# Kernel optimization log

Hardware: AMD Instinct MI355X
Metric: run time of the kernel (lower is better)

The kernel has to match this reference:

```python
import jax, jax.numpy as jnp
import numpy as np

EPS = 1e-6
ROPE_THETA = 10000.0
NH, NKV, HD = 32, 8, 128  # num_heads, num_kv_heads, head_dim


def rmsnorm(x, w):
    # normalize over last dim (head_dim), matching per-head RMSNorm
    return x * jax.lax.rsqrt(jnp.mean(x * x, axis=-1, keepdims=True) + EPS) * w


def rope(x):
    # torchtune-style interleaved RoPE. x: [b, s, h, d]
    b, s, h, d = x.shape
    half = d // 2
    freqs = 1.0 / (ROPE_THETA ** (jnp.arange(0, d, 2, dtype=jnp.float32) / d))  # [d/2]
    ang = jnp.arange(s, dtype=jnp.float32)[:, None] * freqs[None, :]  # [s, d/2]
    cos = jnp.cos(ang)[None, :, None, :]
    sin = jnp.sin(ang)[None, :, None, :]
    xr = x.reshape(b, s, h, half, 2)
    x1, x2 = xr[..., 0], xr[..., 1]
    out = jnp.stack([x1 * cos - x2 * sin, x1 * sin + x2 * cos], axis=-1)
    return out.reshape(b, s, h, d)


def setup_inputs() -> dict:
    key = jax.random.key(0)
    ks = jax.random.split(key, 5)
    b, s, dm = 2, 2048, 4096
    sc = lambda n: 1.0 / np.sqrt(n)
    return {
        "x": jax.random.normal(ks[0], (b, s, dm), jnp.float32),
        "Wq": jax.random.normal(ks[1], (dm, NH * HD), jnp.float32) * sc(dm),
        "Wk": jax.random.normal(ks[2], (dm, NKV * HD), jnp.float32) * sc(dm),
        "Wv": jax.random.normal(ks[3], (dm, NKV * HD), jnp.float32) * sc(dm),
        "Wo": jax.random.normal(ks[4], (NH * HD, dm), jnp.float32) * sc(NH * HD),
        "q_norm_w": jnp.ones((HD,), jnp.float32),
        "k_norm_w": jnp.ones((HD,), jnp.float32),
    }


def reference(x, Wq, Wk, Wv, Wo, q_norm_w, k_norm_w):
    b, s, _ = x.shape
    qpk = NH // NKV  # queries per KV head (GQA groups)
    q = (x @ Wq).reshape(b, s, NH, HD)
    k = (x @ Wk).reshape(b, s, NKV, HD)
    v = (x @ Wv).reshape(b, s, NKV, HD)
    # QK-RMSNorm before RoPE (Qwen3 order)
    q = rope(rmsnorm(q, q_norm_w))
    k = rope(rmsnorm(k, k_norm_w))
    # GQA: group query heads against shared KV heads (no KV materialized expansion)
    q = q.reshape(b, s, NKV, qpk, HD)
    scale = 1.0 / np.sqrt(HD)
    scores = jnp.einsum('bqkgd,bskd->bkgqs', q, k) * scale  # [b, nkv, qpk, s_q, s_k]
    causal = jnp.tril(jnp.ones((s, s), dtype=bool))
    scores = jnp.where(causal[None, None, None], scores, -jnp.inf)
    attn = jax.nn.softmax(scores, axis=-1)
    out = jnp.einsum('bkgqs,bskd->bqkgd', attn, v)  # [b, s_q, nkv, qpk, d]
    return out.reshape(b, s, NH * HD) @ Wo
```

## Files before the change

kernel.cpp:

```cpp
#include <hip/hip_runtime.h>

typedef unsigned short u16;
typedef unsigned int u32;
typedef __attribute__((ext_vector_type(8))) short bf16x8;
typedef __attribute__((ext_vector_type(4))) float f32x4;
typedef __attribute__((ext_vector_type(16))) float f32x16;

#define NH 32
#define NKV 8
#define HD 128
#define SEQ 2048
#define DMODEL 4096
#define QKVN 6144
#define RMS_EPS 1e-6f
#define SM_SCALE 0.08838834764831845f
#define NEG_INF -1e30f

#define AS1 __attribute__((address_space(1)))
#define AS3 __attribute__((address_space(3)))

__device__ __forceinline__ u16 f2bf(float f) {
  unsigned int u = __float_as_uint(f);
  u += 0x7FFFu + ((u >> 16) & 1u);
  return (u16)(u >> 16);
}
__device__ __forceinline__ float bf2f(u16 b) {
  return __uint_as_float(((unsigned int)b) << 16);
}
__device__ __forceinline__ u32 packbf(float lo, float hi) {
  u32 a = __float_as_uint(lo) + 0x8000u;
  u32 b = __float_as_uint(hi) + 0x8000u;
  return __builtin_amdgcn_perm(b, a, 0x07060302u);
}

__device__ __forceinline__ f32x4 mfma16(bf16x8 a, bf16x8 b, f32x4 c) {
  return __builtin_amdgcn_mfma_f32_16x16x32_bf16(a, b, c, 0, 0, 0);
}
__device__ __forceinline__ f32x16 mfma32(bf16x8 a, bf16x8 b, f32x16 c) {
  return __builtin_amdgcn_mfma_f32_32x32x16_bf16(a, b, c, 0, 0, 0);
}

__device__ __forceinline__ void stage16(const u16* g, u16* l) {
  __builtin_amdgcn_global_load_lds((const AS1 u32*)g, (AS3 u32*)l, 16, 0, 0);
}

__global__ __launch_bounds__(256) void cvt_f32_bf16(const float* __restrict__ in,
                                                    u16* __restrict__ out, int n4) {
  int stride = gridDim.x * blockDim.x;
  for (int i = blockIdx.x * blockDim.x + threadIdx.x; i < n4; i += stride) {
    float4 v = ((const float4*)in)[i];
    ushort4 o;
    o.x = f2bf(v.x); o.y = f2bf(v.y); o.z = f2bf(v.z); o.w = f2bf(v.w);
    ((ushort4*)out)[i] = o;
  }
}

__global__ __launch_bounds__(256) void tconv(const float* __restrict__ W, u16* __restrict__ Wt,
                                             int N, int rowoff) {
  __shared__ float t[64][66];
  int n0 = blockIdx.x * 64, k0 = blockIdx.y * 64;
  int tid = threadIdx.x;
  int ln = tid & 63;
  int lk = tid >> 6;
#pragma unroll
  for (int i = 0; i < 16; ++i) {
    int kk = lk + i * 4;
    t[ln][kk] = W[(size_t)(k0 + kk) * N + n0 + ln];
  }
  __syncthreads();
  int kc = tid & 31;
  int nr = tid >> 5;
#pragma unroll
  for (int j = 0; j < 8; ++j) {
    int n = nr + j * 8;
    float2 f = *(const float2*)&t[n][kc * 2];
    ushort2 o;
    o.x = f2bf(f.x);
    o.y = f2bf(f.y);
    *(ushort2*)&Wt[(size_t)(rowoff + n0 + n) * DMODEL + k0 + kc * 2] = o;
  }
}

__device__ __forceinline__ void storeC(u16* p, float v) { *p = f2bf(v); }
__device__ __forceinline__ void storeC(float* p, float v) { *p = v; }

template <typename OutT>
__global__ __launch_bounds__(256) void gemm_sb(const u16* __restrict__ A, const u16* __restrict__ Bt,
                                               OutT* __restrict__ C, int M, int N, int K) {
  __shared__ __align__(16) u16 As[128 * 64];
  __shared__ __align__(16) u16 Bs[128 * 64];
  int nwg = gridDim.x, q8 = nwg >> 3, bid = blockIdx.x;
  int nid = (bid & 7) * q8 + (bid >> 3);
  int mt = M >> 7;
  int m0 = (nid % mt) * 128, n0 = (nid / mt) * 128;
  int tid = threadIdx.x, wave = tid >> 6, lane = tid & 63;
  int wm = (wave >> 1) * 64, wn = (wave & 1) * 64;
  f32x4 acc[4][4] = {};
  int fr = lane & 15, fq = lane >> 4;

  int srow_ = tid >> 3;
  int scol = ((tid & 7) ^ (srow_ & 7)) * 8;
  const u16* aSrc = A + (size_t)(m0 + srow_) * K + scol;
  const u16* bSrc = Bt + (size_t)(n0 + srow_) * K + scol;
  size_t rstride = (size_t)32 * K;
  int dofs = wave * 512;
  int akey = (fr & 7);

  for (int kb = 0; kb < K; kb += 64) {
    __syncthreads();
#pragma unroll
    for (int i = 0; i < 4; ++i) {
      stage16(aSrc + i * rstride + kb, As + i * 2048 + dofs);
      stage16(bSrc + i * rstride + kb, Bs + i * 2048 + dofs);
    }
    __syncthreads();
#pragma unroll
    for (int ks = 0; ks < 2; ++ks) {
      bf16x8 af[4], bfv[4];
      int slot = (ks * 4 + fq) ^ akey;
#pragma unroll
      for (int i = 0; i < 4; ++i)
        af[i] = *(const bf16x8*)((const char*)As + (wm + i * 16 + fr) * 128 + slot * 16);
#pragma unroll
      for (int j = 0; j < 4; ++j)
        bfv[j] = *(const bf16x8*)((const char*)Bs + (wn + j * 16 + fr) * 128 + slot * 16);
      __builtin_amdgcn_s_setprio(1);
#pragma unroll
      for (int i = 0; i < 4; ++i)
#pragma unroll
        for (int j = 0; j < 4; ++j)
          acc[i][j] = mfma16(af[i], bfv[j], acc[i][j]);
      __builtin_amdgcn_s_setprio(0);
    }
  }
#pragma unroll
  for (int i = 0; i < 4; ++i)
#pragma unroll
    for (int j = 0; j < 4; ++j)
#pragma unroll
      for (int r = 0; r < 4; ++r) {
        int row = m0 + wm + i * 16 + fq * 4 + r;
        int col = n0 + wn + j * 16 + fr;
        storeC(&C[(size_t)row * N + col], acc[i][j][r]);
      }
}

template <typename OutT>
__global__ __launch_bounds__(256) void gemm_db(const u16* __restrict__ A, const u16* __restrict__ Bt,
                                               OutT* __restrict__ C, int M, int N, int K) {
  __shared__ __align__(16) u16 As[2][128 * 64];
  __shared__ __align__(16) u16 Bs[2][128 * 64];
  int nwg = gridDim.x, q8 = nwg >> 3, bid = blockIdx.x;
  int nid = (bid & 7) * q8 + (bid >> 3);
  int mt = M >> 7;
  int m0 = (nid % mt) * 128, n0 = (nid / mt) * 128;
  int tid = threadIdx.x, wave = tid >> 6, lane = tid & 63;
  int wm = (wave >> 1) * 64, wn = (wave & 1) * 64;
  f32x4 acc[4][4] = {};
  int fr = lane & 15, fq = lane >> 4;

  int srow_ = tid >> 3;
  int scol = ((tid & 7) ^ (srow_ & 7)) * 8;
  const u16* aSrc = A + (size_t)(m0 + srow_) * K + scol;
  const u16* bSrc = Bt + (size_t)(n0 + srow_) * K + scol;
  size_t rstride = (size_t)32 * K;
  int dofs = wave * 512;
  int akey = (fr & 7);

  auto stage = [&](int buf, int kb) {
#pragma unroll
    for (int i = 0; i < 4; ++i) {
      stage16(aSrc + i * rstride + kb, &As[buf][0] + i * 2048 + dofs);
      stage16(bSrc + i * rstride + kb, &Bs[buf][0] + i * 2048 + dofs);
    }
  };

  int NT = K >> 6;
  stage(0, 0);
  __syncthreads();
  for (int j = 0; j < NT; ++j) {
    int cur = j & 1;
    if (j + 1 < NT) stage(cur ^ 1, (j + 1) << 6);
    const char* Ab = (const char*)&As[cur][0];
    const char* Bb = (const char*)&Bs[cur][0];
#pragma unroll
    for (int ks = 0; ks < 2; ++ks) {
      bf16x8 af[4], bfv[4];
      int slot = (ks * 4 + fq) ^ akey;
#pragma unroll
      for (int i = 0; i < 4; ++i)
        af[i] = *(const bf16x8*)(Ab + (wm + i * 16 + fr) * 128 + slot * 16);
#pragma unroll
      for (int j2 = 0; j2 < 4; ++j2)
        bfv[j2] = *(const bf16x8*)(Bb + (wn + j2 * 16 + fr) * 128 + slot * 16);
      __builtin_amdgcn_s_setprio(1);
#pragma unroll
      for (int i = 0; i < 4; ++i)
#pragma unroll
        for (int j2 = 0; j2 < 4; ++j2)
          acc[i][j2] = mfma16(af[i], bfv[j2], acc[i][j2]);
      __builtin_amdgcn_s_setprio(0);
    }
    __syncthreads();
  }
#pragma unroll
  for (int i = 0; i < 4; ++i)
#pragma unroll
    for (int j = 0; j < 4; ++j)
#pragma unroll
      for (int r = 0; r < 4; ++r) {
        int row = m0 + wm + i * 16 + fq * 4 + r;
        int col = n0 + wn + j * 16 + fr;
        storeC(&C[(size_t)row * N + col], acc[i][j][r]);
      }
}

__global__ __launch_bounds__(256) void normrope(u16* __restrict__ QKV,
                                                const float* __restrict__ qw,
                                                const float* __restrict__ kw) {
  int wq = threadIdx.x >> 6, lane = threadIdx.x & 63;
  int gid = blockIdx.x * 4 + wq;
  int token = gid / 40, head = gid % 40;
  int pos = token & (SEQ - 1);
  const float* wrow;
  int col;
  float sc;
  if (head < NH) { wrow = qw; col = head * HD; sc = SM_SCALE; }
  else           { wrow = kw; col = DMODEL + (head - NH) * HD; sc = 1.0f; }
  u16* row = QKV + (size_t)token * QKVN + col;
  ushort2 xv = *(const ushort2*)(row + 2 * lane);
  float x1 = bf2f(xv.x), x2 = bf2f(xv.y);
  float ssq = x1 * x1 + x2 * x2;
#pragma unroll
  for (int o = 32; o; o >>= 1) ssq += __shfl_xor(ssq, o, 64);
  float rms = rsqrtf(ssq * (1.0f / HD) + RMS_EPS);
  float y1 = x1 * rms * wrow[2 * lane] * sc;
  float y2 = x2 * rms * wrow[2 * lane + 1] * sc;
  float freq = exp2f((float)lane * -0.20762050593046014f);
  float ang = (float)pos * freq;
  float s, c;
  __sincosf(ang, &s, &c);
  ushort2 ov;
  ov.x = f2bf(y1 * c - y2 * s);
  ov.y = f2bf(y1 * s + y2 * c);
  *(ushort2*)(row + 2 * lane) = ov;
}

__global__ __launch_bounds__(512, 2) void attn(const u16* __restrict__ QKV, u16* __restrict__ O) {
  int bid0 = blockIdx.x;
  int bid = (bid0 & 7) * 32 + (bid0 >> 3);
  int pairi = bid & 3, h = (bid >> 2) & 31, b = bid >> 7;
  int tid = threadIdx.x, wave = tid >> 6, lane = tid & 63;
  int qn = lane & 31, hi = lane >> 5;
  int hi4 = hi * 4, hi16 = hi * 16;
  int kvh = h >> 2;

  __shared__ __align__(16) u16 Ks[2][64 * 128];
  __shared__ __align__(16) u16 Vs[2][128 * 64];

  size_t tokb = (size_t)b * SEQ;
  const u16* Kg = QKV + tokb * QKVN + DMODEL + kvh * HD;
  const u16* Vg = Kg + NKV * HD;
  int srow = tid >> 4, sl = tid & 15;

  int kk0 = (qn & 7) << 4;
  int d0 = qn, d1 = 32 + qn, d2 = 64 + qn, d3 = 96 + qn;
  int vk0 = ((d0 ^ (d0 >> 3)) & 7) << 4;
  int vk1 = ((d1 ^ (d1 >> 3)) & 7) << 4;
  int vk2 = ((d2 ^ (d2 >> 3)) & 7) << 4;
  int vk3 = ((d3 ^ (d3 >> 3)) & 7) << 4;

  int4 vreg[2];
  auto loadV = [&](int kv0) {
#pragma unroll
    for (int i = 0; i < 2; ++i)
      vreg[i] = *(const int4*)(Vg + (size_t)(kv0 + i * 32 + srow) * QKVN + sl * 8);
  };
  auto stageK = [&](int buf, int kv0) {
#pragma unroll
    for (int i = 0; i < 2; ++i) {
      int row = i * 32 + srow;
      __builtin_amdgcn_global_load_lds(
          (const AS1 u32*)(Kg + (size_t)(kv0 + row) * QKVN + ((sl ^ (row & 7)) * 8)),
          (AS3 u32*)(&Ks[buf][0] + (i * 32 + wave * 4) * 128), 16, 0, 0);
    }
  };
  auto packV = [&](int buf) {
#pragma unroll
    for (int i = 0; i < 2; ++i) {
      int row = i * 32 + srow;
      int4 dvi = vreg[i];
      int4 dpi;
      dpi.x = __shfl_xor(dvi.x, 16, 64);
      dpi.y = __shfl_xor(dvi.y, 16, 64);
      dpi.z = __shfl_xor(dvi.z, 16, 64);
      dpi.w = __shfl_xor(dvi.w, 16, 64);
      if (((tid >> 4) & 1) == 0) {
        const u16* own = (const u16*)&dvi;
        const u16* par = (const u16*)&dpi;
#pragma unroll
        for (int j = 0; j < 8; ++j) {
          u32 wv = (u32)own[j] | ((u32)par[j] << 16);
          int d = sl * 8 + j;
          int vk = ((d ^ (d >> 3)) & 7) << 4;
          *(u32*)((char*)&Vs[buf][0] + d * 128 + ((2 * row) ^ vk)) = wv;
        }
      }
    }
  };

  for (int pass = 0; pass < 2; ++pass) {
    int chunk = pass ? (7 - pairi) : pairi;
    int chb = chunk * 256;
    int nt = (chunk + 1) * 4;
    int q0w = chb + wave * 32;
    int qabs = q0w + qn;
    int lim = chunk * 4 + (wave >> 1);
    int diag = q0w & ~63;

    bf16x8 qf[8];
    {
      const u16* qp = QKV + (tokb + q0w + qn) * QKVN + h * HD;
#pragma unroll
      for (int d = 0; d < 8; ++d) qf[d] = *(const bf16x8*)(qp + d * 16 + hi * 8);
    }

    f32x16 o0 = {}, o1 = {}, o2 = {}, o3 = {};
    float mrow = NEG_INF, lsum = 0.f;

    auto tile = [&](int kv0, const u16* Kl, const u16* Vl) {
      f32x16 p0v = {}, p1v = {};
      {
        const char* kb0 = (const char*)Kl + qn * 256;
        const char* kb1 = (const char*)Kl + (32 + qn) * 256;
        __builtin_amdgcn_s_setprio(1);
#pragma unroll
        for (int d = 0; d < 8; ++d) {
          bf16x8 k0 = *(const bf16x8*)(kb0 + ((d * 32 + hi16) ^ kk0));
          bf16x8 k1 = *(const bf16x8*)(kb1 + ((d * 32 + hi16) ^ kk0));
          p0v = mfma32(k0, qf[d], p0v);
          p1v = mfma32(k1, qf[d], p1v);
        }
        __builtin_amdgcn_s_setprio(0);
      }
      if (kv0 == diag) {
#pragma unroll
        for (int r = 0; r < 16; ++r) {
          int kva = kv0 + (r & 3) + 8 * (r >> 2) + hi4;
          if (kva > qabs) p0v[r] = NEG_INF;
          if (kva + 32 > qabs) p1v[r] = NEG_INF;
        }
      }
      float tmax = NEG_INF;
#pragma unroll
      for (int r = 0; r < 16; ++r) tmax = fmaxf(tmax, fmaxf(p0v[r], p1v[r]));
      tmax = fmaxf(tmax, __shfl_xor(tmax, 32, 64));
      if (!__all(tmax <= mrow + 8.0f)) {
        float nm = fmaxf(mrow, tmax);
        float corr = __expf(mrow - nm);
        mrow = nm;
        lsum *= corr;
#pragma unroll
        for (int r = 0; r < 16; ++r) {
          int srcl = (r & 3) + 8 * (r >> 2) + hi4;
          float cr = __shfl(corr, srcl, 64);
          o0[r] *= cr; o1[r] *= cr; o2[r] *= cr; o3[r] *= cr;
        }
      }
      float rs = 0.f;
#pragma unroll
      for (int r = 0; r < 16; ++r) {
        p0v[r] = __expf(p0v[r] - mrow);
        p1v[r] = __expf(p1v[r] - mrow);
        rs += p0v[r] + p1v[r];
      }
      rs += __shfl_xor(rs, 32, 64);
      lsum += rs;

      auto pv = [&](const f32x16& pk, int kvs) {
#pragma unroll
        for (int e = 0; e < 2; ++e) {
          u32 A = packbf(pk[e * 8 + 0], pk[e * 8 + 1]);
          u32 Bw = packbf(pk[e * 8 + 2], pk[e * 8 + 3]);
          u32 C = packbf(pk[e * 8 + 4], pk[e * 8 + 5]);
          u32 Dw = packbf(pk[e * 8 + 6], pk[e * 8 + 7]);
          u32 sA = __shfl_xor(A, 32, 64), sC = __shfl_xor(C, 32, 64);
          u32 sB = __shfl_xor(Bw, 32, 64), sD = __shfl_xor(Dw, 32, 64);
          union { u32 w[4]; bf16x8 v; } fr;
          fr.w[0] = hi ? sC : A;
          fr.w[1] = hi ? sD : Bw;
          fr.w[2] = hi ? C : sA;
          fr.w[3] = hi ? Dw : sB;
          int off = (kvs * 2 + e) * 32 + hi16;
          __builtin_amdgcn_s_setprio(1);
          o0 = mfma32(fr.v, *(const bf16x8*)((const char*)Vl + d0 * 128 + (off ^ vk0)), o0);
          o1 = mfma32(fr.v, *(const bf16x8*)((const char*)Vl + d1 * 128 + (off ^ vk1)), o1);
          o2 = mfma32(fr.v, *(const bf16x8*)((const char*)Vl + d2 * 128 + (off ^ vk2)), o2);
          o3 = mfma32(fr.v, *(const bf16x8*)((const char*)Vl + d3 * 128 + (off ^ vk3)), o3);
          __builtin_amdgcn_s_setprio(0);
        }
      };
      pv(p0v, 0);
      pv(p1v, 1);
    };

    loadV(0);
    stageK(0, 0);
    packV(0);
    __syncthreads();

    for (int t = 0; t < nt; ++t) {
      int cur = t & 1, nxt = cur ^ 1;
      bool more = (t + 1) < nt;
      if (more) {
        loadV((t + 1) * 64);
        stageK(nxt, (t + 1) * 64);
      }
      if (t <= lim) tile(t * 64, &Ks[cur][0], &Vs[cur][0]);
      if (more) packV(nxt);
      __syncthreads();
    }

#pragma unroll
    for (int r = 0; r < 16; ++r) {
      int ql = (r & 3) + 8 * (r >> 2) + hi4;
      float ls = __shfl(lsum, ql, 64);
      float inv = 1.0f / ls;
      size_t base = (tokb + chb + wave * 32 + ql) * (size_t)DMODEL + h * HD + qn;
      O[base] = f2bf(o0[r] * inv);
      O[base + 32] = f2bf(o1[r] * inv);
      O[base + 64] = f2bf(o2[r] * inv);
      O[base + 96] = f2bf(o3[r] * inv);
    }
  }
}

extern "C" void kernel_launch(void* const* d_in, const int* in_sizes, int n_in,
                              void* d_out, int out_size, void* d_ws, size_t ws_size,
                              hipStream_t stream) {
  const float* x  = (const float*)d_in[0];
  const float* Wq = (const float*)d_in[1];
  const float* Wk = (const float*)d_in[2];
  const float* Wv = (const float*)d_in[3];
  const float* Wo = (const float*)d_in[4];
  const float* qw = (const float*)d_in[5];
  const float* kw = (const float*)d_in[6];
  float* out = (float*)d_out;

  char* ws = (char*)d_ws;
  u16* xb    = (u16*)(ws);
  u16* Wqkvt = (u16*)(ws + 33554432);
  u16* QKVb  = (u16*)(ws + 83886080);
  u16* Wot   = xb;
  u16* AO    = Wqkvt;

  cvt_f32_bf16<<<2048, 256, 0, stream>>>(x, xb, (2 * SEQ * DMODEL) / 4);
  tconv<<<dim3(DMODEL / 64, DMODEL / 64), 256, 0, stream>>>(Wq, Wqkvt, DMODEL, 0);
  tconv<<<dim3((NKV * HD) / 64, DMODEL / 64), 256, 0, stream>>>(Wk, Wqkvt, NKV * HD, DMODEL);
  tconv<<<dim3((NKV * HD) / 64, DMODEL / 64), 256, 0, stream>>>(Wv, Wqkvt, NKV * HD, DMODEL + NKV * HD);

  gemm_sb<u16><<<(4096 / 128) * (QKVN / 128), 256, 0, stream>>>(xb, Wqkvt, QKVb, 4096, QKVN, DMODEL);
  normrope<<<(4096 * 40) / 4, 256, 0, stream>>>(QKVb, qw, kw);

  tconv<<<dim3(DMODEL / 64, DMODEL / 64), 256, 0, stream>>>(Wo, Wot, DMODEL, 0);
  attn<<<256, 512, 0, stream>>>(QKVb, AO);
  gemm_db<float><<<(4096 / 128) * (DMODEL / 128), 256, 0, stream>>>(AO, Wot, out, 4096, DMODEL, DMODEL);
}
```

Measured before the change: 564.9 us.

## Use double-buffered 128x192 tile GEMM for QKV projection and merge weight conversions

Replaces the single-buffered 128x128 QKV projection GEMM with a double-buffered kernel using 128x192 tiles. Each wave now computes 64x96, and the next K-slice is prefetched while the current one is multiplied, with one barrier per iteration. The grid becomes 32x32 = 1024 blocks, and the three Wq/Wk/Wv transpose-convert launches are merged into one kernel. The changes aim to raise MFMA reuse, hide global-to-LDS latency and cut launch overhead, at the cost of more LDS (80KB) and accumulator registers, which may limit occupancy.

```diff
diff --git a/kernel.cpp b/kernel.cpp
--- a/kernel.cpp
+++ b/kernel.cpp
@@ -55,11 +55,9 @@
   }
 }
 
-__global__ __launch_bounds__(256) void tconv(const float* __restrict__ W, u16* __restrict__ Wt,
-                                             int N, int rowoff) {
+__device__ __forceinline__ void tconv_tile(const float* __restrict__ W, u16* __restrict__ Wt,
+                                           int N, int rowoff, int n0, int k0, int tid) {
   __shared__ float t[64][66];
-  int n0 = blockIdx.x * 64, k0 = blockIdx.y * 64;
-  int tid = threadIdx.x;
   int ln = tid & 63;
   int lk = tid >> 6;
 #pragma unroll
@@ -81,21 +79,37 @@
   }
 }
 
+__global__ __launch_bounds__(256) void tconv3(const float* __restrict__ Wq,
+                                              const float* __restrict__ Wk,
+                                              const float* __restrict__ Wv,
+                                              u16* __restrict__ Wt) {
+  int bx = blockIdx.x, k0 = blockIdx.y * 64, tid = threadIdx.x;
+  if (bx < 64)       tconv_tile(Wq, Wt, DMODEL, 0, bx * 64, k0, tid);
+  else if (bx < 80)  tconv_tile(Wk, Wt, NKV * HD, DMODEL, (bx - 64) * 64, k0, tid);
+  else               tconv_tile(Wv, Wt, NKV * HD, DMODEL + NKV * HD, (bx - 80) * 64, k0, tid);
+}
+
+__global__ __launch_bounds__(256) void tconv(const float* __restrict__ W, u16* __restrict__ Wt,
+                                             int N, int rowoff) {
+  tconv_tile(W, Wt, N, rowoff, blockIdx.x * 64, blockIdx.y * 64, threadIdx.x);
+}
+
 __device__ __forceinline__ void storeC(u16* p, float v) { *p = f2bf(v); }
 __device__ __forceinline__ void storeC(float* p, float v) { *p = v; }
 
 template <typename OutT>
-__global__ __launch_bounds__(256) void gemm_sb(const u16* __restrict__ A, const u16* __restrict__ Bt,
-                                               OutT* __restrict__ C, int M, int N, int K) {
-  __shared__ __align__(16) u16 As[128 * 64];
-  __shared__ __align__(16) u16 Bs[128 * 64];
+__global__ __launch_bounds__(256, 2) void gemm_db192(const u16* __restrict__ A,
+                                                     const u16* __restrict__ Bt,
+                                                     OutT* __restrict__ C, int M, int N, int K) {
+  __shared__ __align__(16) u16 As[2][128 * 64];
+  __shared__ __align__(16) u16 Bs[2][192 * 64];
   int nwg = gridDim.x, q8 = nwg >> 3, bid = blockIdx.x;
   int nid = (bid & 7) * q8 + (bid >> 3);
   int mt = M >> 7;
-  int m0 = (nid % mt) * 128, n0 = (nid / mt) * 128;
+  int m0 = (nid % mt) * 128, n0 = (nid / mt) * 192;
   int tid = threadIdx.x, wave = tid >> 6, lane = tid & 63;
-  int wm = (wave >> 1) * 64, wn = (wave & 1) * 64;
-  f32x4 acc[4][4] = {};
+  int wm = (wave >> 1) * 64, wn = (wave & 1) * 96;
+  f32x4 acc[4][6] = {};
   int fr = lane & 15, fq = lane >> 4;
 
   int srow_ = tid >> 3;
@@ -106,37 +120,47 @@
   int dofs = wave * 512;
   int akey = (fr & 7);
 
-  for (int kb = 0; kb < K; kb += 64) {
+  auto stage = [&](int buf, int kb) {
+#pragma unroll
+    for (int i = 0; i < 4; ++i)
+      stage16(aSrc + i * rstride + kb, &As[buf][0] + i * 2048 + dofs);
+#pragma unroll
+    for (int i = 0; i < 6; ++i)
+      stage16(bSrc + i * rstride + kb, &Bs[buf][0] + i * 2048 + dofs);
+  };
+
+  int NT = K >> 6;
+  stage(0, 0);
+  __syncthreads();
+  for (int j = 0; j < NT; ++j) {
+    int cur = j & 1;
+    if (j + 1 < NT) stage(cur ^ 1, (j + 1) << 6);
+    const char* Ab = (const char*)&As[cur][0];
+    const char* Bb = (const char*)&Bs[cur][0];
+#pragma unroll
+    for (int ks = 0; ks < 2; ++ks) {
+      bf16x8 af[4], bfv[6];
+      int slot = (ks * 4 + fq) ^ akey;
+#pragma unroll
+      for (int i = 0; i < 4; ++i)
+        af[i] = *(const bf16x8*)(Ab + (wm + i * 16 + fr) * 128 + slot * 16);
+#pragma unroll
+      for (int j2 = 0; j2 < 6; ++j2)
+        bfv[j2] = *(const bf16x8*)(Bb + (wn + j2 * 16 + fr) * 128 + slot * 16);
+      __builtin_amdgcn_s_setprio(1);
+#pragma unroll
+      for (int i = 0; i < 4; ++i)
+#pragma unroll
+        for (int j2 = 0; j2 < 6; ++j2)
+          acc[i][j2] = mfma16(af[i], bfv[j2], acc[i][j2]);
+      __builtin_amdgcn_s_setprio(0);
+    }
     __syncthreads();
-#pragma unroll
-    for (int i = 0; i < 4; ++i) {
-      stage16(aSrc + i * rstride + kb, As + i * 2048 + dofs);
-      stage16(bSrc + i * rstride + kb, Bs + i * 2048 + dofs);
-    }
-    __syncthreads();
-#pragma unroll
-    for (int ks = 0; ks < 2; ++ks) {
-      bf16x8 af[4], bfv[4];
-      int slot = (ks * 4 + fq) ^ akey;
-#pragma unroll
-      for (int i = 0; i < 4; ++i)
-        af[i] = *(const bf16x8*)((const char*)As + (wm + i * 16 + fr) * 128 + slot * 16);
-#pragma unroll
-      for (int j = 0; j < 4; ++j)
-        bfv[j] = *(const bf16x8*)((const char*)Bs + (wn + j * 16 + fr) * 128 + slot * 16);
-      __builtin_amdgcn_s_setprio(1);
-#pragma unroll
-      for (int i = 0; i < 4; ++i)
-#pragma unroll
-        for (int j = 0; j < 4; ++j)
-          acc[i][j] = mfma16(af[i], bfv[j], acc[i][j]);
-      __builtin_amdgcn_s_setprio(0);
-    }
   }
 #pragma unroll
   for (int i = 0; i < 4; ++i)
 #pragma unroll
-    for (int j = 0; j < 4; ++j)
+    for (int j = 0; j < 6; ++j)
 #pragma unroll
       for (int r = 0; r < 4; ++r) {
         int row = m0 + wm + i * 16 + fq * 4 + r;
@@ -455,11 +479,9 @@
   u16* AO    = Wqkvt;
 
   cvt_f32_bf16<<<2048, 256, 0, stream>>>(x, xb, (2 * SEQ * DMODEL) / 4);
-  tconv<<<dim3(DMODEL / 64, DMODEL / 64), 256, 0, stream>>>(Wq, Wqkvt, DMODEL, 0);
-  tconv<<<dim3((NKV * HD) / 64, DMODEL / 64), 256, 0, stream>>>(Wk, Wqkvt, NKV * HD, DMODEL);
-  tconv<<<dim3((NKV * HD) / 64, DMODEL / 64), 256, 0, stream>>>(Wv, Wqkvt, NKV * HD, DMODEL + NKV * HD);
-
-  gemm_sb<u16><<<(4096 / 128) * (QKVN / 128), 256, 0, stream>>>(xb, Wqkvt, QKVb, 4096, QKVN, DMODEL);
+  tconv3<<<dim3(96, DMODEL / 64), 256, 0, stream>>>(Wq, Wk, Wv, Wqkvt);
+
+  gemm_db192<u16><<<(4096 / 128) * (QKVN / 192), 256, 0, stream>>>(xb, Wqkvt, QKVb, 4096, QKVN, DMODEL);
   normrope<<<(4096 * 40) / 4, 256, 0, stream>>>(QKVb, qw, kw);
 
   tconv<<<dim3(DMODEL / 64, DMODEL / 64), 256, 0, stream>>>(Wo, Wot, DMODEL, 0);
```

Result: faster. 549.3 us (-2.8%).
